# Kernel tuning notes

Hardware: AMD Instinct MI355X
Metric: run time of the kernel (lower is better)

The kernel has to match this reference:

```python
import jax, jax.numpy as jnp
import numpy as np

EMBED_DIMS = [8, 16, 8]      # prod = 1024 = embed_dim
HIDDEN_DIMS = [16, 16, 16]   # prod = 4096 = hidden_dim
RANK = 16
B, S = 4, 1024


def _make_cores(key, in_dims, out_dims, rank):
    d = len(in_dims)
    ranks = [1] + [rank] * (d - 1) + [1]
    cores = []
    for k in range(d):
        key, sub = jax.random.split(key)
        shape = (ranks[k], in_dims[k], out_dims[k], ranks[k + 1])
        scale = 1.0 / np.sqrt(in_dims[k] * ranks[k])
        cores.append((scale * jax.random.normal(sub, shape, dtype=jnp.float32)))
    return cores


def setup_inputs() -> dict:
    key = jax.random.key(0)
    k_x, k1, k2, kb1, kb2 = jax.random.split(key, 5)
    x = jax.random.normal(k_x, (B, S, 1024), dtype=jnp.float32)
    fc1 = _make_cores(k1, EMBED_DIMS, HIDDEN_DIMS, RANK)
    fc2 = _make_cores(k2, HIDDEN_DIMS, EMBED_DIMS, RANK)
    b1 = 0.01 * jax.random.normal(kb1, (4096,), dtype=jnp.float32)
    b2 = 0.01 * jax.random.normal(kb2, (1024,), dtype=jnp.float32)
    return {
        "x": x,
        "fc1_c0": fc1[0], "fc1_c1": fc1[1], "fc1_c2": fc1[2], "fc1_b": b1,
        "fc2_c0": fc2[0], "fc2_c1": fc2[1], "fc2_c2": fc2[2], "fc2_b": b2,
    }


def tt_linear(x_flat, cores, bias, in_dims):
    """TT-matrix x batch-of-vectors product. x_flat: [N, prod(in_dims)].

    Cores: core_k has shape [r_{k-1}, n_k, m_k, r_k] with r_0 = r_d = 1.
    Invariant: acc is [r_{k-1}, n_k, rest] with rest laid out as
    (n_{k+1}..n_d, N, m_1..m_{k-1}).
    """
    N = x_flat.shape[0]
    acc = x_flat.reshape((N,) + tuple(in_dims))      # [N, n1..nd]
    acc = jnp.moveaxis(acc, 0, -1)                   # [n1..nd, N]
    acc = acc.reshape(in_dims[0], -1)[None]          # [1, n1, rest]
    d = len(cores)
    for k, c in enumerate(cores):
        # contract previous rank + current input mode
        acc = jnp.einsum('pnR,pnmq->Rmq', acc, c)    # [rest, m_k, r_k]
        if k < d - 1:
            n_next = in_dims[k + 1]
            R, m, q = acc.shape
            acc = acc.reshape(n_next, R // n_next, m, q)
            acc = jnp.transpose(acc, (3, 0, 1, 2)).reshape(q, n_next, -1)
    # final acc: [N * m1..m_{d-1}, m_d, 1] -> [N, M]
    return acc.reshape(N, -1) + bias


def reference(x, fc1_c0, fc1_c1, fc1_c2, fc1_b, fc2_c0, fc2_c1, fc2_c2, fc2_b):
    flat = x.reshape(-1, x.shape[-1])                        # [N, embed_dim]
    z1 = tt_linear(flat, [fc1_c0, fc1_c1, fc1_c2], fc1_b, EMBED_DIMS)   # [N, hidden]
    h1 = jax.nn.gelu(z1, approximate=False)                  # exact erf GELU (torch default)
    z2 = tt_linear(h1, [fc2_c0, fc2_c1, fc2_c2], fc2_b, HIDDEN_DIMS)    # [N, embed]
    return z2.reshape(*x.shape[:-1], z2.shape[-1])
```

## Files before the change

kernel.cpp:

```cpp
#include <hip/hip_runtime.h>
#include <stdint.h>

__device__ __forceinline__ float b2f(unsigned short u) {
    union { uint32_t i; float f; } v; v.i = ((uint32_t)u) << 16; return v.f;
}
__device__ __forceinline__ unsigned short f2b(float f) {
    union { float f; uint32_t i; } v; v.f = f;
    uint32_t r = v.i + 0x7fffu + ((v.i >> 16) & 1u);
    return (unsigned short)(r >> 16);
}

typedef __bf16 bf16x8 __attribute__((ext_vector_type(8)));
typedef float  f32x16 __attribute__((ext_vector_type(16)));

__global__ __launch_bounds__(256)
void cvt_f32_bf16(const float* __restrict__ x, unsigned short* __restrict__ xb) {
    int t = blockIdx.x * 256 + threadIdx.x;
    const float4* p = (const float4*)(x + (size_t)t * 8);
    float4 f0 = p[0], f1 = p[1];
    int4 o;
    o.x = (uint32_t)f2b(f0.x) | ((uint32_t)f2b(f0.y) << 16);
    o.y = (uint32_t)f2b(f0.z) | ((uint32_t)f2b(f0.w) << 16);
    o.z = (uint32_t)f2b(f1.x) | ((uint32_t)f2b(f1.y) << 16);
    o.w = (uint32_t)f2b(f1.z) | ((uint32_t)f2b(f1.w) << 16);
    ((int4*)xb)[t] = o;
}

template<int N3, int M3>
__global__ void build_T(const float* __restrict__ c1,
                        const float* __restrict__ c2,
                        float* __restrict__ T) {
    int e = blockIdx.x * 256 + threadIdx.x;
    int m3 = e % M3;
    int t  = e / M3;
    int n3 = t % N3;
    int rm = t / N3;
    float s = 0.f;
#pragma unroll
    for (int r2 = 0; r2 < 16; ++r2)
        s += c1[rm * 16 + r2] * c2[(r2 * N3 + n3) * M3 + m3];
    T[e] = s;
}

template<int N1, int N2, int N3, int M1, int M2, int M3>
__global__ __launch_bounds__(256)
void build_W(const float* __restrict__ c0,
             const float* __restrict__ T,
             unsigned short* __restrict__ W) {
    constexpr int K = N1 * N2 * N3;
    int t  = blockIdx.x * 256 + threadIdx.x;
    int m3 = t % M3;
    int m2 = (t / M3) % M2;
    int n2 = (t / (M3 * M2)) % N2;
    int m1 = (t / (M3 * M2 * N2)) % M1;
    int n1 =  t / (M3 * M2 * N2 * M1);

    float c0r[16];
    const float4* c0p = (const float4*)(c0 + (n1 * M1 + m1) * 16);
#pragma unroll
    for (int i = 0; i < 4; ++i) ((float4*)c0r)[i] = c0p[i];

    float acc[N3] = {};
#pragma unroll
    for (int r1 = 0; r1 < 16; ++r1) {
        const float* Tp = T + (size_t)(((r1 * 16 + n2) * 16 + m2) * N3) * M3 + m3;
#pragma unroll
        for (int n3 = 0; n3 < N3; ++n3)
            acc[n3] += c0r[r1] * Tp[n3 * M3];
    }

    unsigned short ob[N3];
#pragma unroll
    for (int n3 = 0; n3 < N3; ++n3) ob[n3] = f2b(acc[n3]);

    unsigned short* dst = W + (size_t)((m1 * M2 + m2) * M3 + m3) * K
                            + (n1 * N2 + n2) * N3;
#pragma unroll
    for (int c = 0; c < N3 / 8; ++c)
        ((int4*)dst)[c] = ((const int4*)ob)[c];
}

#define PC_COMPUTE(BUF)                                                       \
    {                                                                         \
        _Pragma("unroll")                                                     \
        for (int ks = 0; ks < 4; ++ks) {                                      \
            bf16x8 a_f[FI], b_f[FJ];                                          \
            _Pragma("unroll")                                                 \
            for (int i = 0; i < FI; ++i) {                                    \
                const int key = (m32 & 7) ^                                   \
                    (((waveM >> 3) + 4 * i + (m32 >> 3)) & 7);                \
                const int slot = ((ks * 2 + khalf) ^ key) * 8;                \
                a_f[i] = *(const bf16x8*)&As[(BUF) * ASZ +                    \
                          (waveM + i * 32 + m32) * BK + slot];                \
            }                                                                 \
            _Pragma("unroll")                                                 \
            for (int j = 0; j < FJ; ++j) {                                    \
                const int key = (m32 & 7) ^                                   \
                    (((waveN >> 3) + 4 * j + (m32 >> 3)) & 7);                \
                const int slot = ((ks * 2 + khalf) ^ key) * 8;                \
                b_f[j] = *(const bf16x8*)&Bs[(BUF) * BSZ +                    \
                          (waveN + j * 32 + m32) * BK + slot];                \
            }                                                                 \
            _Pragma("unroll")                                                 \
            for (int i = 0; i < FI; ++i)                                      \
                _Pragma("unroll")                                             \
                for (int j = 0; j < FJ; ++j)                                  \
                    acc[i][j] = __builtin_amdgcn_mfma_f32_32x32x16_bf16(      \
                        a_f[i], b_f[j], acc[i][j], 0, 0, 0);                  \
        }                                                                     \
    }

template<int BM, int BN, int KTOT, bool DO_GELU, bool A_F32, bool C_F32>
__global__ __launch_bounds__(512, 4)
void gemm_pc(const void* __restrict__ Av,
             const unsigned short* __restrict__ Bt,
             const float* __restrict__ bias,
             void* __restrict__ Cv,
             int Ncols) {
    constexpr int BK  = 64;
    constexpr int CA  = BM / 8;
    constexpr int CB  = BN / 8;
    constexpr int PA  = CA / 4;
    constexpr int PB  = CB / 4;
    constexpr int FI  = BM / 64;
    constexpr int FJ  = BN / 64;
    constexpr int ASZ = BM * BK;
    constexpr int BSZ = BN * BK;
    __shared__ unsigned short As[2 * ASZ];
    __shared__ unsigned short Bs[2 * BSZ];

    const int tid  = threadIdx.x;
    const int lane = tid & 63;
    const int wave = tid >> 6;
    const int rowBase = blockIdx.y * BM;
    const int colBase = blockIdx.x * BN;

    const int lr    = lane >> 3;
    const int jj    = lane & 7;
    const int m32   = lane & 31;
    const int khalf = lane >> 5;

    if (wave >= 4) {
        const int pw = wave - 4;

#pragma unroll
        for (int it = 0; it < PA; ++it) {
            const int c  = pw * PA + it;
            const int jg = jj ^ lr ^ (c & 7);
            const size_t aoff = (size_t)(rowBase + c * 8 + lr) * KTOT + jg * 8;
            int4 v;
            if (A_F32) {
                const float* ga = (const float*)Av + aoff;
                float4 f0 = *(const float4*)ga;
                float4 f1 = *(const float4*)(ga + 4);
                v.x = (uint32_t)f2b(f0.x) | ((uint32_t)f2b(f0.y) << 16);
                v.y = (uint32_t)f2b(f0.z) | ((uint32_t)f2b(f0.w) << 16);
                v.z = (uint32_t)f2b(f1.x) | ((uint32_t)f2b(f1.y) << 16);
                v.w = (uint32_t)f2b(f1.z) | ((uint32_t)f2b(f1.w) << 16);
            } else {
                v = *(const int4*)((const unsigned short*)Av + aoff);
            }
            *(int4*)&As[c * 512 + lane * 8] = v;
        }
#pragma unroll
        for (int it = 0; it < PB; ++it) {
            const int c  = pw * PB + it;
            const int jg = jj ^ lr ^ (c & 7);
            *(int4*)&Bs[c * 512 + lane * 8] =
                *(const int4*)(Bt + (size_t)(colBase + c * 8 + lr) * KTOT + jg * 8);
        }
        __syncthreads();

        int buf = 1;
        for (int k0 = BK; k0 < KTOT; k0 += BK) {
            int4 aR[PA], bR[PB];
#pragma unroll
            for (int it = 0; it < PA; ++it) {
                const int c  = pw * PA + it;
                const int jg = jj ^ lr ^ (c & 7);
                const size_t aoff = (size_t)(rowBase + c * 8 + lr) * KTOT + k0 + jg * 8;
                if (A_F32) {
                    const float* ga = (const float*)Av + aoff;
                    float4 f0 = *(const float4*)ga;
                    float4 f1 = *(const float4*)(ga + 4);
                    int4 v;
                    v.x = (uint32_t)f2b(f0.x) | ((uint32_t)f2b(f0.y) << 16);
                    v.y = (uint32_t)f2b(f0.z) | ((uint32_t)f2b(f0.w) << 16);
                    v.z = (uint32_t)f2b(f1.x) | ((uint32_t)f2b(f1.y) << 16);
                    v.w = (uint32_t)f2b(f1.z) | ((uint32_t)f2b(f1.w) << 16);
                    aR[it] = v;
                } else {
                    aR[it] = *(const int4*)((const unsigned short*)Av + aoff);
                }
            }
#pragma unroll
            for (int it = 0; it < PB; ++it) {
                const int c  = pw * PB + it;
                const int jg = jj ^ lr ^ (c & 7);
                bR[it] = *(const int4*)(Bt + (size_t)(colBase + c * 8 + lr) * KTOT + k0 + jg * 8);
            }
#pragma unroll
            for (int it = 0; it < PA; ++it) {
                const int c = pw * PA + it;
                *(int4*)&As[buf * ASZ + c * 512 + lane * 8] = aR[it];
            }
#pragma unroll
            for (int it = 0; it < PB; ++it) {
                const int c = pw * PB + it;
                *(int4*)&Bs[buf * BSZ + c * 512 + lane * 8] = bR[it];
            }
            __syncthreads();
            buf ^= 1;
        }
    } else {
        const int waveM = (wave >> 1) * (BM / 2);
        const int waveN = (wave & 1) * (BN / 2);
        f32x16 acc[FI][FJ] = {};

        __syncthreads();

        int cur = 0;
        for (int k0 = BK; k0 < KTOT; k0 += BK) {
            PC_COMPUTE(cur)
            __syncthreads();
            cur ^= 1;
        }
        PC_COMPUTE(cur)

#pragma unroll
        for (int i = 0; i < FI; ++i) {
#pragma unroll
            for (int j = 0; j < FJ; ++j) {
                const int col = colBase + waveN + j * 32 + m32;
                const float bv = bias[col];
#pragma unroll
                for (int reg = 0; reg < 16; ++reg) {
                    const int row = rowBase + waveM + i * 32 +
                                    (reg & 3) + 8 * (reg >> 2) + 4 * khalf;
                    float z = acc[i][j][reg] + bv;
                    if (DO_GELU)
                        z = 0.5f * z * (1.f + erff(z * 0.70710678118654752f));
                    const size_t off = (size_t)row * Ncols + col;
                    if (C_F32) ((float*)Cv)[off] = z;
                    else       ((unsigned short*)Cv)[off] = f2b(z);
                }
            }
        }
    }
}

extern "C" void kernel_launch(void* const* d_in, const int* in_sizes, int n_in,
                              void* d_out, int out_size, void* d_ws, size_t ws_size,
                              hipStream_t stream) {
    const float* x      = (const float*)d_in[0];
    const float* fc1_c0 = (const float*)d_in[1];
    const float* fc1_c1 = (const float*)d_in[2];
    const float* fc1_c2 = (const float*)d_in[3];
    const float* fc1_b  = (const float*)d_in[4];
    const float* fc2_c0 = (const float*)d_in[5];
    const float* fc2_c1 = (const float*)d_in[6];
    const float* fc2_c2 = (const float*)d_in[7];
    const float* fc2_b  = (const float*)d_in[8];

    char* ws = (char*)d_ws;
    unsigned short* W  = (unsigned short*)(ws);
    float*          T  = (float*)(ws + (8u << 20));
    const bool big = ws_size >= (50ull << 20);
    unsigned short* xb = (unsigned short*)(ws + (10u << 20));
    unsigned short* h  = (unsigned short*)(ws + (big ? (18u << 20) : (10u << 20)));

    build_T<8, 16><<<2048, 256, 0, stream>>>(fc1_c1, fc1_c2, T);
    build_W<8, 16, 8, 16, 16, 16><<<2048, 256, 0, stream>>>(fc1_c0, T, W);
    if (big) {
        cvt_f32_bf16<<<2048, 256, 0, stream>>>(x, xb);
        gemm_pc<128, 128, 1024, true, false, false>
            <<<dim3(32, 32), 512, 0, stream>>>(xb, W, fc1_b, h, 4096);
    } else {
        gemm_pc<128, 128, 1024, true, true, false>
            <<<dim3(32, 32), 512, 0, stream>>>(x, W, fc1_b, h, 4096);
    }

    build_T<16, 8><<<2048, 256, 0, stream>>>(fc2_c1, fc2_c2, T);
    build_W<16, 16, 16, 8, 16, 8><<<1024, 256, 0, stream>>>(fc2_c0, T, W);
    gemm_pc<128, 64, 4096, false, false, true>
        <<<dim3(16, 32), 512, 0, stream>>>(h, W, fc2_b, d_out, 1024);
}
```

Measured before the change: 229.2 us.

## Replace producer-consumer GEMMs with triple-buffered direct-to-LDS async-load GEMM

Adds a new GEMM kernel that stages A and B tiles straight into LDS through global_load_lds, using a three-deep ring buffer with loads issued two K-tiles ahead. All eight waves now compute instead of splitting into producer and consumer waves, and the kernel uses larger tiles (256x128 for fc1, 128x128 for fc2), a swizzled block order, and raised MFMA priority. The aim is to hide global memory latency and make better use of the matrix units. The cost is more dynamic shared memory per block, which may limit occupancy, plus a static one-time attribute setup on the host.

Result: slower. 237.5 us (+3.6%).

```diff
diff --git a/kernel.cpp b/kernel.cpp
--- a/kernel.cpp
+++ b/kernel.cpp
@@ -78,6 +78,156 @@
 #pragma unroll
     for (int c = 0; c < N3 / 8; ++c)
         ((int4*)dst)[c] = ((const int4*)ob)[c];
+}
+
+template<int BM, int BN>
+__device__ __forceinline__ void stage_chunk16(
+    const unsigned short* __restrict__ A,
+    const unsigned short* __restrict__ Bt,
+    char* __restrict__ dstbuf, int ktot,
+    int rowBase, int colBase, int tk, int c, int tid)
+{
+    const int off  = (c * 512 + tid) * 16;
+    const bool isB = off >= BM * 128;
+    const int off2 = isB ? off - BM * 128 : off;
+    const int r    = off2 >> 7;
+    const int jg   = ((off2 >> 4) & 7) ^ (r & 7);
+    const unsigned short* src = (isB ? Bt + (size_t)(colBase + r) * ktot
+                                     : A  + (size_t)(rowBase + r) * ktot)
+                                + tk * 64 + jg * 8;
+    void* dst = dstbuf + (c * 8192 + (tid >> 6) * 1024);
+    __builtin_amdgcn_global_load_lds(
+        (const __attribute__((address_space(1))) void*)src,
+        (__attribute__((address_space(3))) void*)dst, 16, 0, 0);
+}
+
+template<int BM, int BN, int KTOT, int NCOLS, int PPT, bool DO_GELU, bool C_F32>
+__global__ __launch_bounds__(512, 2)
+void gemm3p(const unsigned short* __restrict__ A,
+            const unsigned short* __restrict__ Bt,
+            const float* __restrict__ bias,
+            void* __restrict__ Cv)
+{
+    constexpr int BK   = 64;
+    constexpr int NT   = KTOT / BK;
+    constexpr int BUFB = (BM + BN) * 128;
+    constexpr int LPT  = (BM + BN) * BK * 2 / (512 * 16);
+    constexpr int SPP  = LPT / PPT;
+    constexpr int KPP  = 4 / PPT;
+    constexpr int WGM  = 4, WGN = 2;
+    constexpr int FI   = BM / (WGM * 32);
+    constexpr int FJ   = BN / (WGN * 32);
+    constexpr int GX   = NCOLS / BN;
+
+    extern __shared__ char smem[];
+
+    const int tid  = threadIdx.x;
+    const int lane = tid & 63;
+    const int wave = tid >> 6;
+    const int m32  = lane & 31;
+    const int kh   = lane >> 5;
+    const int wm   = wave >> 1;
+    const int wn   = wave & 1;
+
+    int lin = blockIdx.y * GX + blockIdx.x;
+    const int cpx = (int)(GX * gridDim.y) >> 3;
+    lin = (lin & 7) * cpx + (lin >> 3);
+    const int rowBase = (lin / GX) * BM;
+    const int colBase = (lin % GX) * BN;
+
+    f32x16 acc[FI][FJ] = {};
+
+#pragma unroll
+    for (int c = 0; c < LPT; ++c)
+        stage_chunk16<BM, BN>(A, Bt, smem, KTOT, rowBase, colBase, 0, c, tid);
+#pragma unroll
+    for (int c = 0; c < LPT; ++c)
+        stage_chunk16<BM, BN>(A, Bt, smem + BUFB, KTOT, rowBase, colBase, 1, c, tid);
+    asm volatile("s_waitcnt vmcnt(%0)" :: "n"(LPT) : "memory");
+    __builtin_amdgcn_s_barrier();
+    asm volatile("" ::: "memory");
+
+    int bt = 0;
+    for (int t = 0; t < NT; ++t) {
+        const int sb = bt >= 1 ? bt - 1 : 2;
+        const char* Ab = smem + bt * BUFB;
+        const char* Bb = Ab + BM * 128;
+        char* Sb = smem + sb * BUFB;
+        const bool doStage = (t + 2 < NT);
+
+#pragma unroll
+        for (int ph = 0; ph < PPT; ++ph) {
+            bf16x8 af[FI][KPP], bfr[FJ][KPP];
+#pragma unroll
+            for (int i = 0; i < FI; ++i) {
+                const int rr = wm * (BM / WGM) + i * 32 + m32;
+#pragma unroll
+                for (int u = 0; u < KPP; ++u) {
+                    const int lc = (ph * KPP + u) * 2 + kh;
+                    af[i][u] = *(const bf16x8*)(Ab + rr * 128 + ((lc ^ (rr & 7)) << 4));
+                }
+            }
+#pragma unroll
+            for (int j = 0; j < FJ; ++j) {
+                const int rr = wn * (BN / WGN) + j * 32 + m32;
+#pragma unroll
+                for (int u = 0; u < KPP; ++u) {
+                    const int lc = (ph * KPP + u) * 2 + kh;
+                    bfr[j][u] = *(const bf16x8*)(Bb + rr * 128 + ((lc ^ (rr & 7)) << 4));
+                }
+            }
+            if (doStage) {
+#pragma unroll
+                for (int c = 0; c < SPP; ++c)
+                    stage_chunk16<BM, BN>(A, Bt, Sb, KTOT, rowBase, colBase,
+                                          t + 2, ph * SPP + c, tid);
+            }
+            __builtin_amdgcn_s_barrier();
+            asm volatile("s_waitcnt lgkmcnt(0)" ::: "memory");
+            __builtin_amdgcn_s_setprio(1);
+#pragma unroll
+            for (int u = 0; u < KPP; ++u)
+#pragma unroll
+                for (int i = 0; i < FI; ++i)
+#pragma unroll
+                    for (int j = 0; j < FJ; ++j)
+                        acc[i][j] = __builtin_amdgcn_mfma_f32_32x32x16_bf16(
+                            af[i][u], bfr[j][u], acc[i][j], 0, 0, 0);
+            __builtin_amdgcn_s_setprio(0);
+            if (ph == PPT - 1) {
+                if (t + 2 < NT) {
+                    asm volatile("s_waitcnt vmcnt(%0)" :: "n"(LPT) : "memory");
+                } else if (t + 1 < NT) {
+                    asm volatile("s_waitcnt vmcnt(0)" ::: "memory");
+                }
+            }
+            __builtin_amdgcn_s_barrier();
+            asm volatile("" ::: "memory");
+        }
+        bt = bt < 2 ? bt + 1 : 0;
+    }
+
+    const int waveM = wm * (BM / WGM);
+    const int waveN = wn * (BN / WGN);
+#pragma unroll
+    for (int i = 0; i < FI; ++i) {
+#pragma unroll
+        for (int j = 0; j < FJ; ++j) {
+            const int col = colBase + waveN + j * 32 + m32;
+            const float bv = bias[col];
+#pragma unroll
+            for (int reg = 0; reg < 16; ++reg) {
+                const int row = rowBase + waveM + i * 32 +
+                                (reg & 3) + 8 * (reg >> 2) + 4 * kh;
+                float z = acc[i][j][reg] + bv;
+                if (DO_GELU)
+                    z = 0.5f * z * (1.f + erff(z * 0.70710678118654752f));
+                const size_t off = (size_t)row * NCOLS + col;
+                if (C_F32) ((float*)Cv)[off] = z;
+                else       ((unsigned short*)Cv)[off] = f2b(z);
+            }
+        }
+    }
 }
 
 #define PC_COMPUTE(BUF)                                                       \
@@ -142,7 +292,6 @@
 
     if (wave >= 4) {
         const int pw = wave - 4;
-
 #pragma unroll
         for (int it = 0; it < PA; ++it) {
             const int c  = pw * PA + it;
@@ -269,12 +418,23 @@
     unsigned short* xb = (unsigned short*)(ws + (10u << 20));
     unsigned short* h  = (unsigned short*)(ws + (big ? (18u << 20) : (10u << 20)));
 
+    static bool attr_done = false;
+    if (!attr_done) {
+        attr_done = true;
+        (void)hipFuncSetAttribute(
+            reinterpret_cast<const void*>(&gemm3p<256, 128, 1024, 4096, 2, true, false>),
+            hipFuncAttributeMaxDynamicSharedMemorySize, 3 * (256 + 128) * 128);
+        (void)hipFuncSetAttribute(
+            reinterpret_cast<const void*>(&gemm3p<128, 128, 4096, 1024, 1, false, true>),
+            hipFuncAttributeMaxDynamicSharedMemorySize, 3 * (128 + 128) * 128);
+    }
+
     build_T<8, 16><<<2048, 256, 0, stream>>>(fc1_c1, fc1_c2, T);
     build_W<8, 16, 8, 16, 16, 16><<<2048, 256, 0, stream>>>(fc1_c0, T, W);
     if (big) {
         cvt_f32_bf16<<<2048, 256, 0, stream>>>(x, xb);
-        gemm_pc<128, 128, 1024, true, false, false>
-            <<<dim3(32, 32), 512, 0, stream>>>(xb, W, fc1_b, h, 4096);
+        gemm3p<256, 128, 1024, 4096, 2, true, false>
+            <<<dim3(32, 16), 512, 3 * (256 + 128) * 128, stream>>>(xb, W, fc1_b, h);
     } else {
         gemm_pc<128, 128, 1024, true, true, false>
             <<<dim3(32, 32), 512, 0, stream>>>(x, W, fc1_b, h, 4096);
@@ -282,6 +442,6 @@
 
     build_T<16, 8><<<2048, 256, 0, stream>>>(fc2_c1, fc2_c2, T);
     build_W<16, 16, 16, 8, 16, 8><<<1024, 256, 0, stream>>>(fc2_c0, T, W);
-    gemm_pc<128, 64, 4096, false, false, true>
-        <<<dim3(16, 32), 512, 0, stream>>>(h, W, fc2_b, d_out, 1024);
-}
+    gemm3p<128, 128, 4096, 1024, 1, false, true>
+        <<<dim3(8, 32), 512, 3 * (128 + 128) * 128, stream>>>(h, W, fc2_b, d_out);
+}
```

## Add larger-tile producer/consumer GEMM with split-K atomics for second layer

Applied to the files above, without the earlier changes.

Adds a new warp-specialized GEMM kernel with 256x128 tiles, dynamic LDS double buffering, register-staged prefetch of two K-steps, and an XCD-aware block remap. The first GEMM uses it with fused GELU. The second GEMM is split across K into two chunks that accumulate with atomic adds into an output pre-filled with bias by a new kernel. This targets better data reuse and more parallelism for the narrow second GEMM, at the cost of atomic traffic, an extra launch, and nondeterministic summation order.

Measured after the change: 445.0 us. 1.94x slower.

```diff
diff --git a/kernel.cpp b/kernel.cpp
--- a/kernel.cpp
+++ b/kernel.cpp
@@ -24,6 +24,12 @@
     o.z = (uint32_t)f2b(f1.x) | ((uint32_t)f2b(f1.y) << 16);
     o.w = (uint32_t)f2b(f1.z) | ((uint32_t)f2b(f1.w) << 16);
     ((int4*)xb)[t] = o;
+}
+
+__global__ __launch_bounds__(256)
+void bias_fill(const float* __restrict__ b, float4* __restrict__ out) {
+    int t = blockIdx.x * 256 + threadIdx.x;
+    out[t] = ((const float4*)b)[t & 255];
 }
 
 template<int N3, int M3>
@@ -78,6 +84,157 @@
 #pragma unroll
     for (int c = 0; c < N3 / 8; ++c)
         ((int4*)dst)[c] = ((const int4*)ob)[c];
+}
+
+template<int BM, int BN, int KCH, int NCOLS, int GX, int GY,
+         bool DO_GELU, bool ATOMIC>
+__global__ __launch_bounds__(512, 2)
+void gemm_pc2(const unsigned short* __restrict__ A,
+              const unsigned short* __restrict__ Bt,
+              const float* __restrict__ bias,
+              void* __restrict__ Cv,
+              int kstride)
+{
+    constexpr int BK  = 64;
+    constexpr int NT  = KCH / BK;
+    constexpr int CA  = BM / 8, CB = BN / 8;
+    constexpr int PA  = CA / 4, PB = CB / 4;
+    constexpr int ASZ = BM * BK, BSZ = BN * BK;
+    constexpr int BUFE = ASZ + BSZ;
+
+    extern __shared__ unsigned short sh[];
+
+    const int tid   = threadIdx.x;
+    const int lane  = tid & 63;
+    const int wave  = tid >> 6;
+    const int lr    = lane >> 3;
+    const int jj    = lane & 7;
+    const int m32   = lane & 31;
+    const int khalf = lane >> 5;
+
+    int lin = ((int)blockIdx.z * GY + (int)blockIdx.y) * GX + (int)blockIdx.x;
+    const int total = GX * GY * (int)gridDim.z;
+    const int cpx = total >> 3;
+    lin = (lin & 7) * cpx + (lin >> 3);
+    const int colT = lin % GX;
+    const int rowT = (lin / GX) % GY;
+    const int kz   = lin / (GX * GY);
+    const int rowBase = rowT * BM;
+    const int colBase = colT * BN;
+    const int kOff    = kz * KCH;
+
+    if (wave >= 4) {
+        const int pw = wave - 4;
+        int4 rA0[PA], rB0[PB];
+        int4 rA1[PA], rB1[PB];
+
+        auto LOADP = [&](int4 (&aR)[PA], int4 (&bR)[PB], int t) {
+            const int kk = kOff + t * BK;
+#pragma unroll
+            for (int it = 0; it < PA; ++it) {
+                const int c  = pw * PA + it;
+                const int jg = jj ^ lr ^ (c & 7);
+                aR[it] = *(const int4*)(A +
+                    (size_t)(rowBase + c * 8 + lr) * kstride + kk + jg * 8);
+            }
+#pragma unroll
+            for (int it = 0; it < PB; ++it) {
+                const int c  = pw * PB + it;
+                const int jg = jj ^ lr ^ (c & 7);
+                bR[it] = *(const int4*)(Bt +
+                    (size_t)(colBase + c * 8 + lr) * kstride + kk + jg * 8);
+            }
+        };
+        auto STOREP = [&](int4 (&aR)[PA], int4 (&bR)[PB], int b) {
+            unsigned short* As = sh + b * BUFE;
+            unsigned short* Bs = As + ASZ;
+#pragma unroll
+            for (int it = 0; it < PA; ++it)
+                *(int4*)&As[(pw * PA + it) * 512 + lane * 8] = aR[it];
+#pragma unroll
+            for (int it = 0; it < PB; ++it)
+                *(int4*)&Bs[(pw * PB + it) * 512 + lane * 8] = bR[it];
+        };
+
+        LOADP(rA0, rB0, 0);
+        LOADP(rA1, rB1, 1);
+        STOREP(rA0, rB0, 0);
+        __syncthreads();
+
+        for (int t = 0; t < NT; t += 2) {
+            if (t + 2 < NT) LOADP(rA0, rB0, t + 2);
+            STOREP(rA1, rB1, 1);
+            __syncthreads();
+            if (t + 3 < NT) LOADP(rA1, rB1, t + 3);
+            if (t + 2 < NT) STOREP(rA0, rB0, 0);
+            __syncthreads();
+        }
+    } else {
+        const int wm = wave >> 1, wn = wave & 1;
+        const int waveM = wm * 128, waveN = wn * 64;
+        f32x16 acc[4][2] = {};
+
+        int aAddr[4], aKey[4], bAddr[2], bKey[2];
+#pragma unroll
+        for (int i = 0; i < 4; ++i) {
+            const int r = waveM + i * 32 + m32;
+            aAddr[i] = r * BK;
+            aKey[i]  = (r & 7) ^ ((r >> 3) & 7);
+        }
+#pragma unroll
+        for (int j = 0; j < 2; ++j) {
+            const int r = waveN + j * 32 + m32;
+            bAddr[j] = ASZ + r * BK;
+            bKey[j]  = (r & 7) ^ ((r >> 3) & 7);
+        }
+
+        __syncthreads();
+
+        for (int t = 0; t < NT; ++t) {
+            const unsigned short* base = sh + (t & 1) * BUFE;
+#pragma unroll
+            for (int ks = 0; ks < 4; ++ks) {
+                bf16x8 a_f[4], b_f[2];
+                const int g = ks * 2 + khalf;
+#pragma unroll
+                for (int i = 0; i < 4; ++i)
+                    a_f[i] = *(const bf16x8*)&base[aAddr[i] + (g ^ aKey[i]) * 8];
+#pragma unroll
+                for (int j = 0; j < 2; ++j)
+                    b_f[j] = *(const bf16x8*)&base[bAddr[j] + (g ^ bKey[j]) * 8];
+#pragma unroll
+                for (int i = 0; i < 4; ++i)
+#pragma unroll
+                    for (int j = 0; j < 2; ++j)
+                        acc[i][j] = __builtin_amdgcn_mfma_f32_32x32x16_bf16(
+                            a_f[i], b_f[j], acc[i][j], 0, 0, 0);
+            }
+            __syncthreads();
+        }
+
+#pragma unroll
+        for (int i = 0; i < 4; ++i) {
+#pragma unroll
+            for (int j = 0; j < 2; ++j) {
+                const int col = colBase + waveN + j * 32 + m32;
+                const float bv = ATOMIC ? 0.f : bias[col];
+#pragma unroll
+                for (int reg = 0; reg < 16; ++reg) {
+                    const int row = rowBase + waveM + i * 32 +
+                                    (reg & 3) + 8 * (reg >> 2) + 4 * khalf;
+                    const size_t off = (size_t)row * NCOLS + col;
+                    if (ATOMIC) {
+                        unsafeAtomicAdd((float*)Cv + off, acc[i][j][reg]);
+                    } else {
+                        float z = acc[i][j][reg] + bv;
+                        if (DO_GELU)
+                            z = 0.5f * z * (1.f + erff(z * 0.70710678118654752f));
+                        ((unsigned short*)Cv)[off] = f2b(z);
+                    }
+                }
+            }
+        }
+    }
 }
 
 #define PC_COMPUTE(BUF)                                                       \
@@ -142,7 +299,6 @@
 
     if (wave >= 4) {
         const int pw = wave - 4;
-
 #pragma unroll
         for (int it = 0; it < PA; ++it) {
             const int c  = pw * PA + it;
@@ -269,12 +425,27 @@
     unsigned short* xb = (unsigned short*)(ws + (10u << 20));
     unsigned short* h  = (unsigned short*)(ws + (big ? (18u << 20) : (10u << 20)));
 
+    constexpr int DLDS = 2 * (256 + 128) * 64 * 2;
+
+    static bool attr_done = false;
+    if (!attr_done) {
+        attr_done = true;
+        (void)hipFuncSetAttribute(
+            reinterpret_cast<const void*>(
+                &gemm_pc2<256, 128, 1024, 4096, 32, 16, true, false>),
+            hipFuncAttributeMaxDynamicSharedMemorySize, DLDS);
+        (void)hipFuncSetAttribute(
+            reinterpret_cast<const void*>(
+                &gemm_pc2<256, 128, 2048, 1024, 8, 16, false, true>),
+            hipFuncAttributeMaxDynamicSharedMemorySize, DLDS);
+    }
+
     build_T<8, 16><<<2048, 256, 0, stream>>>(fc1_c1, fc1_c2, T);
     build_W<8, 16, 8, 16, 16, 16><<<2048, 256, 0, stream>>>(fc1_c0, T, W);
     if (big) {
         cvt_f32_bf16<<<2048, 256, 0, stream>>>(x, xb);
-        gemm_pc<128, 128, 1024, true, false, false>
-            <<<dim3(32, 32), 512, 0, stream>>>(xb, W, fc1_b, h, 4096);
+        gemm_pc2<256, 128, 1024, 4096, 32, 16, true, false>
+            <<<dim3(32, 16, 1), 512, DLDS, stream>>>(xb, W, fc1_b, h, 1024);
     } else {
         gemm_pc<128, 128, 1024, true, true, false>
             <<<dim3(32, 32), 512, 0, stream>>>(x, W, fc1_b, h, 4096);
@@ -282,6 +453,12 @@
 
     build_T<16, 8><<<2048, 256, 0, stream>>>(fc2_c1, fc2_c2, T);
     build_W<16, 16, 16, 8, 16, 8><<<1024, 256, 0, stream>>>(fc2_c0, T, W);
-    gemm_pc<128, 64, 4096, false, false, true>
-        <<<dim3(16, 32), 512, 0, stream>>>(h, W, fc2_b, d_out, 1024);
-}
+    if (big) {
+        bias_fill<<<4096, 256, 0, stream>>>(fc2_b, (float4*)d_out);
+        gemm_pc2<256, 128, 2048, 1024, 8, 16, false, true>
+            <<<dim3(8, 16, 2), 512, DLDS, stream>>>(h, W, fc2_b, d_out, 4096);
+    } else {
+        gemm_pc<128, 64, 4096, false, false, true>
+            <<<dim3(16, 32), 512, 0, stream>>>(h, W, fc2_b, d_out, 1024);
+    }
+}
```

## Merge weight-build kernels, fuse x conversion, deepen producer prefetch pipeline

Applied to the files above, without the earlier changes.

The two build_T launches and the two build_W launches are each merged into a single kernel, and T scratch moves into the output buffer. The separate f32-to-bf16 conversion kernel is dropped, so the first GEMM reads fp32 x directly. The producer waves in the GEMM now keep one tile of global loads in flight while storing the previous tile to LDS, which deepens the prefetch. The swizzle key computation is also simplified. The goal is fewer launches and better hiding of global-load latency, at the cost of more producer registers and extra fp32 reads of x.

Result: slower. 301.9 us (+31.7%).

```diff
diff --git a/kernel.cpp b/kernel.cpp
--- a/kernel.cpp
+++ b/kernel.cpp
@@ -13,24 +13,11 @@
 typedef __bf16 bf16x8 __attribute__((ext_vector_type(8)));
 typedef float  f32x16 __attribute__((ext_vector_type(16)));
 
-__global__ __launch_bounds__(256)
-void cvt_f32_bf16(const float* __restrict__ x, unsigned short* __restrict__ xb) {
-    int t = blockIdx.x * 256 + threadIdx.x;
-    const float4* p = (const float4*)(x + (size_t)t * 8);
-    float4 f0 = p[0], f1 = p[1];
-    int4 o;
-    o.x = (uint32_t)f2b(f0.x) | ((uint32_t)f2b(f0.y) << 16);
-    o.y = (uint32_t)f2b(f0.z) | ((uint32_t)f2b(f0.w) << 16);
-    o.z = (uint32_t)f2b(f1.x) | ((uint32_t)f2b(f1.y) << 16);
-    o.w = (uint32_t)f2b(f1.z) | ((uint32_t)f2b(f1.w) << 16);
-    ((int4*)xb)[t] = o;
-}
-
 template<int N3, int M3>
-__global__ void build_T(const float* __restrict__ c1,
-                        const float* __restrict__ c2,
-                        float* __restrict__ T) {
-    int e = blockIdx.x * 256 + threadIdx.x;
+__device__ __forceinline__ void build_T_body(int e,
+                                             const float* __restrict__ c1,
+                                             const float* __restrict__ c2,
+                                             float* __restrict__ T) {
     int m3 = e % M3;
     int t  = e / M3;
     int n3 = t % N3;
@@ -42,13 +29,22 @@
     T[e] = s;
 }
 
+__global__ __launch_bounds__(256)
+void build_T_both(const float* __restrict__ c11, const float* __restrict__ c12,
+                  float* __restrict__ T1,
+                  const float* __restrict__ c21, const float* __restrict__ c22,
+                  float* __restrict__ T2) {
+    const int b = blockIdx.x;
+    if (b < 2048) build_T_body<8, 16>(b * 256 + threadIdx.x, c11, c12, T1);
+    else          build_T_body<16, 8>((b - 2048) * 256 + threadIdx.x, c21, c22, T2);
+}
+
 template<int N1, int N2, int N3, int M1, int M2, int M3>
-__global__ __launch_bounds__(256)
-void build_W(const float* __restrict__ c0,
-             const float* __restrict__ T,
-             unsigned short* __restrict__ W) {
+__device__ __forceinline__ void build_W_body(int t,
+                                             const float* __restrict__ c0,
+                                             const float* __restrict__ T,
+                                             unsigned short* __restrict__ W) {
     constexpr int K = N1 * N2 * N3;
-    int t  = blockIdx.x * 256 + threadIdx.x;
     int m3 = t % M3;
     int m2 = (t / M3) % M2;
     int n2 = (t / (M3 * M2)) % N2;
@@ -80,152 +76,153 @@
         ((int4*)dst)[c] = ((const int4*)ob)[c];
 }
 
-#define PC_COMPUTE(BUF)                                                       \
-    {                                                                         \
-        _Pragma("unroll")                                                     \
-        for (int ks = 0; ks < 4; ++ks) {                                      \
-            bf16x8 a_f[FI], b_f[FJ];                                          \
-            _Pragma("unroll")                                                 \
-            for (int i = 0; i < FI; ++i) {                                    \
-                const int key = (m32 & 7) ^                                   \
-                    (((waveM >> 3) + 4 * i + (m32 >> 3)) & 7);                \
-                const int slot = ((ks * 2 + khalf) ^ key) * 8;                \
-                a_f[i] = *(const bf16x8*)&As[(BUF) * ASZ +                    \
-                          (waveM + i * 32 + m32) * BK + slot];                \
-            }                                                                 \
-            _Pragma("unroll")                                                 \
-            for (int j = 0; j < FJ; ++j) {                                    \
-                const int key = (m32 & 7) ^                                   \
-                    (((waveN >> 3) + 4 * j + (m32 >> 3)) & 7);                \
-                const int slot = ((ks * 2 + khalf) ^ key) * 8;                \
-                b_f[j] = *(const bf16x8*)&Bs[(BUF) * BSZ +                    \
-                          (waveN + j * 32 + m32) * BK + slot];                \
-            }                                                                 \
-            _Pragma("unroll")                                                 \
-            for (int i = 0; i < FI; ++i)                                      \
-                _Pragma("unroll")                                             \
-                for (int j = 0; j < FJ; ++j)                                  \
-                    acc[i][j] = __builtin_amdgcn_mfma_f32_32x32x16_bf16(      \
-                        a_f[i], b_f[j], acc[i][j], 0, 0, 0);                  \
-        }                                                                     \
-    }
+__global__ __launch_bounds__(256)
+void build_W_both(const float* __restrict__ c10, const float* __restrict__ T1,
+                  unsigned short* __restrict__ W1,
+                  const float* __restrict__ c20, const float* __restrict__ T2,
+                  unsigned short* __restrict__ W2) {
+    const int b = blockIdx.x;
+    if (b < 2048)
+        build_W_body<8, 16, 8, 16, 16, 16>(b * 256 + threadIdx.x, c10, T1, W1);
+    else
+        build_W_body<16, 16, 16, 8, 16, 8>((b - 2048) * 256 + threadIdx.x, c20, T2, W2);
+}
+
+template<int N1, int N2, int N3, int M1, int M2, int M3>
+__global__ __launch_bounds__(256)
+void build_W(const float* __restrict__ c0, const float* __restrict__ T,
+             unsigned short* __restrict__ W) {
+    build_W_body<N1, N2, N3, M1, M2, M3>(blockIdx.x * 256 + threadIdx.x, c0, T, W);
+}
 
 template<int BM, int BN, int KTOT, bool DO_GELU, bool A_F32, bool C_F32>
 __global__ __launch_bounds__(512, 4)
-void gemm_pc(const void* __restrict__ Av,
-             const unsigned short* __restrict__ Bt,
-             const float* __restrict__ bias,
-             void* __restrict__ Cv,
-             int Ncols) {
+void gemm_pc3(const void* __restrict__ Av,
+              const unsigned short* __restrict__ Bt,
+              const float* __restrict__ bias,
+              void* __restrict__ Cv,
+              int Ncols)
+{
     constexpr int BK  = 64;
-    constexpr int CA  = BM / 8;
-    constexpr int CB  = BN / 8;
-    constexpr int PA  = CA / 4;
-    constexpr int PB  = CB / 4;
-    constexpr int FI  = BM / 64;
-    constexpr int FJ  = BN / 64;
-    constexpr int ASZ = BM * BK;
-    constexpr int BSZ = BN * BK;
+    constexpr int NT  = KTOT / BK;
+    constexpr int CA  = BM / 8, CB = BN / 8;
+    constexpr int PA  = CA / 4, PB = CB / 4;
+    constexpr int FI  = BM / 64, FJ = BN / 64;
+    constexpr int ASZ = BM * BK, BSZ = BN * BK;
     __shared__ unsigned short As[2 * ASZ];
     __shared__ unsigned short Bs[2 * BSZ];
 
-    const int tid  = threadIdx.x;
-    const int lane = tid & 63;
-    const int wave = tid >> 6;
-    const int rowBase = blockIdx.y * BM;
-    const int colBase = blockIdx.x * BN;
-
+    const int tid   = threadIdx.x;
+    const int lane  = tid & 63;
+    const int wave  = tid >> 6;
     const int lr    = lane >> 3;
     const int jj    = lane & 7;
     const int m32   = lane & 31;
     const int khalf = lane >> 5;
+    const int rowBase = blockIdx.y * BM;
+    const int colBase = blockIdx.x * BN;
 
     if (wave >= 4) {
         const int pw = wave - 4;
-
-#pragma unroll
-        for (int it = 0; it < PA; ++it) {
-            const int c  = pw * PA + it;
-            const int jg = jj ^ lr ^ (c & 7);
-            const size_t aoff = (size_t)(rowBase + c * 8 + lr) * KTOT + jg * 8;
-            int4 v;
-            if (A_F32) {
-                const float* ga = (const float*)Av + aoff;
-                float4 f0 = *(const float4*)ga;
-                float4 f1 = *(const float4*)(ga + 4);
-                v.x = (uint32_t)f2b(f0.x) | ((uint32_t)f2b(f0.y) << 16);
-                v.y = (uint32_t)f2b(f0.z) | ((uint32_t)f2b(f0.w) << 16);
-                v.z = (uint32_t)f2b(f1.x) | ((uint32_t)f2b(f1.y) << 16);
-                v.w = (uint32_t)f2b(f1.z) | ((uint32_t)f2b(f1.w) << 16);
-            } else {
-                v = *(const int4*)((const unsigned short*)Av + aoff);
-            }
-            *(int4*)&As[c * 512 + lane * 8] = v;
+        float4 aF[PA][2];
+        int4   aR[PA];
+        int4   bR[PB];
+
+#define PC3_LOAD(T_)                                                          \
+        { const int kk = (T_) * BK;                                           \
+          _Pragma("unroll")                                                   \
+          for (int it = 0; it < PA; ++it) {                                   \
+              const int c  = pw * PA + it;                                    \
+              const int jg = jj ^ lr ^ (c & 7);                               \
+              const size_t aoff = (size_t)(rowBase + c * 8 + lr) * KTOT       \
+                                  + kk + jg * 8;                              \
+              if constexpr (A_F32) {                                          \
+                  const float* ga = (const float*)Av + aoff;                  \
+                  aF[it][0] = *(const float4*)ga;                             \
+                  aF[it][1] = *(const float4*)(ga + 4);                       \
+              } else {                                                        \
+                  aR[it] = *(const int4*)((const unsigned short*)Av + aoff);  \
+              }                                                               \
+          }                                                                   \
+          _Pragma("unroll")                                                   \
+          for (int it = 0; it < PB; ++it) {                                   \
+              const int c  = pw * PB + it;                                    \
+              const int jg = jj ^ lr ^ (c & 7);                               \
+              bR[it] = *(const int4*)(Bt +                                    \
+                  (size_t)(colBase + c * 8 + lr) * KTOT + kk + jg * 8);       \
+          } }
+
+#define PC3_STORE(B_)                                                         \
+        { unsigned short* As_ = As + (B_) * ASZ;                              \
+          unsigned short* Bs_ = Bs + (B_) * BSZ;                              \
+          _Pragma("unroll")                                                   \
+          for (int it = 0; it < PA; ++it) {                                   \
+              int4 v;                                                         \
+              if constexpr (A_F32) {                                          \
+                  v.x = (uint32_t)f2b(aF[it][0].x) |                          \
+                        ((uint32_t)f2b(aF[it][0].y) << 16);                   \
+                  v.y = (uint32_t)f2b(aF[it][0].z) |                          \
+                        ((uint32_t)f2b(aF[it][0].w) << 16);                   \
+                  v.z = (uint32_t)f2b(aF[it][1].x) |                          \
+                        ((uint32_t)f2b(aF[it][1].y) << 16);                   \
+                  v.w = (uint32_t)f2b(aF[it][1].z) |                          \
+                        ((uint32_t)f2b(aF[it][1].w) << 16);                   \
+              } else {                                                        \
+                  v = aR[it];                                                 \
+              }                                                               \
+              *(int4*)&As_[(pw * PA + it) * 512 + lane * 8] = v;              \
+          }                                                                   \
+          _Pragma("unroll")                                                   \
+          for (int it = 0; it < PB; ++it)                                     \
+              *(int4*)&Bs_[(pw * PB + it) * 512 + lane * 8] = bR[it]; }
+
+        PC3_LOAD(0)
+        PC3_STORE(0)
+        PC3_LOAD(1)
+        __syncthreads();
+
+        for (int t = 0; t < NT; ++t) {
+            if (t + 1 < NT) PC3_STORE((t + 1) & 1)
+            if (t + 2 < NT) PC3_LOAD(t + 2)
+            __syncthreads();
         }
-#pragma unroll
-        for (int it = 0; it < PB; ++it) {
-            const int c  = pw * PB + it;
-            const int jg = jj ^ lr ^ (c & 7);
-            *(int4*)&Bs[c * 512 + lane * 8] =
-                *(const int4*)(Bt + (size_t)(colBase + c * 8 + lr) * KTOT + jg * 8);
-        }
+#undef PC3_LOAD
+#undef PC3_STORE
+    } else {
+        const int wm = wave >> 1, wn = wave & 1;
+        const int waveM = wm * (BM / 2), waveN = wn * (BN / 2);
+        f32x16 acc[FI][FJ] = {};
+
         __syncthreads();
 
-        int buf = 1;
-        for (int k0 = BK; k0 < KTOT; k0 += BK) {
-            int4 aR[PA], bR[PB];
-#pragma unroll
-            for (int it = 0; it < PA; ++it) {
-                const int c  = pw * PA + it;
-                const int jg = jj ^ lr ^ (c & 7);
-                const size_t aoff = (size_t)(rowBase + c * 8 + lr) * KTOT + k0 + jg * 8;
-                if (A_F32) {
-                    const float* ga = (const float*)Av + aoff;
-                    float4 f0 = *(const float4*)ga;
-                    float4 f1 = *(const float4*)(ga + 4);
-                    int4 v;
-                    v.x = (uint32_t)f2b(f0.x) | ((uint32_t)f2b(f0.y) << 16);
-                    v.y = (uint32_t)f2b(f0.z) | ((uint32_t)f2b(f0.w) << 16);
-                    v.z = (uint32_t)f2b(f1.x) | ((uint32_t)f2b(f1.y) << 16);
-                    v.w = (uint32_t)f2b(f1.z) | ((uint32_t)f2b(f1.w) << 16);
-                    aR[it] = v;
-                } else {
-                    aR[it] = *(const int4*)((const unsigned short*)Av + aoff);
+        for (int t = 0; t < NT; ++t) {
+            const unsigned short* Ab = As + (t & 1) * ASZ;
+            const unsigned short* Bb = Bs + (t & 1) * BSZ;
+#pragma unroll
+            for (int ks = 0; ks < 4; ++ks) {
+                bf16x8 a_f[FI], b_f[FJ];
+                const int g = ks * 2 + khalf;
+#pragma unroll
+                for (int i = 0; i < FI; ++i) {
+                    const int r = waveM + i * 32 + m32;
+                    const int key = (r & 7) ^ ((r >> 3) & 7);
+                    a_f[i] = *(const bf16x8*)&Ab[r * BK + ((g ^ key) << 3)];
                 }
-            }
-#pragma unroll
-            for (int it = 0; it < PB; ++it) {
-                const int c  = pw * PB + it;
-                const int jg = jj ^ lr ^ (c & 7);
-                bR[it] = *(const int4*)(Bt + (size_t)(colBase + c * 8 + lr) * KTOT + k0 + jg * 8);
-            }
-#pragma unroll
-            for (int it = 0; it < PA; ++it) {
-                const int c = pw * PA + it;
-                *(int4*)&As[buf * ASZ + c * 512 + lane * 8] = aR[it];
-            }
-#pragma unroll
-            for (int it = 0; it < PB; ++it) {
-                const int c = pw * PB + it;
-                *(int4*)&Bs[buf * BSZ + c * 512 + lane * 8] = bR[it];
+#pragma unroll
+                for (int j = 0; j < FJ; ++j) {
+                    const int r = waveN + j * 32 + m32;
+                    const int key = (r & 7) ^ ((r >> 3) & 7);
+                    b_f[j] = *(const bf16x8*)&Bb[r * BK + ((g ^ key) << 3)];
+                }
+#pragma unroll
+                for (int i = 0; i < FI; ++i)
+#pragma unroll
+                    for (int j = 0; j < FJ; ++j)
+                        acc[i][j] = __builtin_amdgcn_mfma_f32_32x32x16_bf16(
+                            a_f[i], b_f[j], acc[i][j], 0, 0, 0);
             }
             __syncthreads();
-            buf ^= 1;
         }
-    } else {
-        const int waveM = (wave >> 1) * (BM / 2);
-        const int waveN = (wave & 1) * (BN / 2);
-        f32x16 acc[FI][FJ] = {};
-
-        __syncthreads();
-
-        int cur = 0;
-        for (int k0 = BK; k0 < KTOT; k0 += BK) {
-            PC_COMPUTE(cur)
-            __syncthreads();
-            cur ^= 1;
-        }
-        PC_COMPUTE(cur)
 
 #pragma unroll
         for (int i = 0; i < FI; ++i) {
@@ -262,26 +259,35 @@
     const float* fc2_c2 = (const float*)d_in[7];
     const float* fc2_b  = (const float*)d_in[8];
 
+    float* T1 = (float*)d_out;
+    float* T2 = (float*)d_out + 524288;
+
     char* ws = (char*)d_ws;
-    unsigned short* W  = (unsigned short*)(ws);
-    float*          T  = (float*)(ws + (8u << 20));
-    const bool big = ws_size >= (50ull << 20);
-    unsigned short* xb = (unsigned short*)(ws + (10u << 20));
-    unsigned short* h  = (unsigned short*)(ws + (big ? (18u << 20) : (10u << 20)));
-
-    build_T<8, 16><<<2048, 256, 0, stream>>>(fc1_c1, fc1_c2, T);
-    build_W<8, 16, 8, 16, 16, 16><<<2048, 256, 0, stream>>>(fc1_c0, T, W);
+    const bool big = ws_size >= (48ull << 20);
+
+    build_T_both<<<4096, 256, 0, stream>>>(fc1_c1, fc1_c2, T1,
+                                           fc2_c1, fc2_c2, T2);
+
     if (big) {
-        cvt_f32_bf16<<<2048, 256, 0, stream>>>(x, xb);
-        gemm_pc<128, 128, 1024, true, false, false>
-            <<<dim3(32, 32), 512, 0, stream>>>(xb, W, fc1_b, h, 4096);
+        unsigned short* W1 = (unsigned short*)ws;
+        unsigned short* W2 = (unsigned short*)(ws + (8u << 20));
+        unsigned short* h  = (unsigned short*)(ws + (16u << 20));
+
+        build_W_both<<<3072, 256, 0, stream>>>(fc1_c0, T1, W1,
+                                               fc2_c0, T2, W2);
+        gemm_pc3<128, 128, 1024, true, true, false>
+            <<<dim3(32, 32), 512, 0, stream>>>(x, W1, fc1_b, h, 4096);
+        gemm_pc3<128, 64, 4096, false, false, true>
+            <<<dim3(16, 32), 512, 0, stream>>>(h, W2, fc2_b, d_out, 1024);
     } else {
-        gemm_pc<128, 128, 1024, true, true, false>
+        unsigned short* W = (unsigned short*)ws;
+        unsigned short* h = (unsigned short*)(ws + (8u << 20));
+
+        build_W<8, 16, 8, 16, 16, 16><<<2048, 256, 0, stream>>>(fc1_c0, T1, W);
+        gemm_pc3<128, 128, 1024, true, true, false>
             <<<dim3(32, 32), 512, 0, stream>>>(x, W, fc1_b, h, 4096);
+        build_W<16, 16, 16, 8, 16, 8><<<1024, 256, 0, stream>>>(fc2_c0, T2, W);
+        gemm_pc3<128, 64, 4096, false, false, true>
+            <<<dim3(16, 32), 512, 0, stream>>>(h, W, fc2_b, d_out, 1024);
     }
-
-    build_T<16, 8><<<2048, 256, 0, stream>>>(fc2_c1, fc2_c2, T);
-    build_W<16, 16, 16, 8, 16, 8><<<1024, 256, 0, stream>>>(fc2_c0, T, W);
-    gemm_pc<128, 64, 4096, false, false, true>
-        <<<dim3(16, 32), 512, 0, stream>>>(h, W, fc2_b, d_out, 1024);
-}
+}
```
